# Performance work log

Measured on AMD Instinct MI355X. Metric: run time of the kernel, lower is better.

The kernel has to match this reference:

```python
import jax, jax.numpy as jnp
import numpy as np

B, S, D, H, E, K = 4, 1024, 1024, 4096, 8, 2

def setup_inputs() -> dict:
    key = jax.random.key(0)
    ks = jax.random.split(key, 6)
    sd = 1.0 / np.sqrt(D)
    sh = 1.0 / np.sqrt(H)
    return {
        "x": jax.random.normal(ks[0], (B, S, D), jnp.float32),
        "Wg": jax.random.normal(ks[1], (D, E), jnp.float32) * sd,
        "bg": jnp.zeros((E,), jnp.float32),
        "W1": jax.random.normal(ks[2], (E, D, H), jnp.float32) * sd,
        "b1": jnp.zeros((E, H), jnp.float32),
        "Wa": jax.random.normal(ks[3], (E, D, H), jnp.float32) * sd,
        "ba": jnp.zeros((E, H), jnp.float32),
        "W2": jax.random.normal(ks[4], (E, H, D), jnp.float32) * sh,
        "b2": jnp.zeros((E, D), jnp.float32),
        "kv_cache": 0,
    }

def reference(x, Wg, bg, W1, b1, Wa, ba, W2, b2, kv_cache):
    # gate: softmax over experts, top-k, renormalize
    gate = jax.nn.softmax(x @ Wg + bg, axis=-1)            # [B,S,E]
    w, idx = jax.lax.top_k(gate, K)                        # [B,S,K]
    w = w / jnp.sum(w, axis=-1, keepdims=True)
    # dense all-expert FF with SwiGLU: fc2( silu(fc_a(x)) * fc1(x) )
    a = jnp.einsum('bsd,edh->bseh', x, Wa) + ba            # [B,S,E,H]
    g = a * jax.nn.sigmoid(a)
    u = jnp.einsum('bsd,edh->bseh', x, W1) + b1
    y = jnp.einsum('bseh,ehd->bsed', g * u, W2) + b2       # [B,S,E,D]
    # gather top-k experts per token and combine
    sel = jnp.take_along_axis(y, idx[..., None], axis=2)   # [B,S,K,D]
    out = jnp.sum(sel * w[..., None], axis=-2)             # [B,S,D]
    return out
```

## Files before the change

kernel.cpp:

```cpp
#include <hip/hip_runtime.h>
#include <hip/hip_bf16.h>
#include <math.h>

#define TOKENS 4096
#define DD 1024
#define HH 4096
#define NE 8
#define PAIRS 8192
#define ROWCAP 8448
#define TILE_CAP 40

typedef __bf16 bf16x8 __attribute__((ext_vector_type(8)));
typedef float f32x4 __attribute__((ext_vector_type(4)));

__device__ __forceinline__ unsigned short f2bf(float f) {
  union { float f; unsigned int u; } c; c.f = f;
  unsigned int x = c.u;
  return (unsigned short)((x + 0x7fffu + ((x >> 16) & 1u)) >> 16);
}

__device__ __forceinline__ void lds16(void* l, const void* g) {
  __builtin_amdgcn_global_load_lds((const __attribute__((address_space(1))) void*)g,
                                   (__attribute__((address_space(3))) void*)l, 16, 0, 0);
}

__global__ void init_kernel(int* counts) {
  if (threadIdx.x < NE) counts[threadIdx.x] = 0;
}

__global__ __launch_bounds__(256) void transpose_kernel(const float* __restrict__ in,
                                                        unsigned short* __restrict__ out,
                                                        int R, int C) {
  int ntr = R >> 6, ntc = C >> 6;
  int per_e = ntr * ntc;
  int b = blockIdx.x;
  int e = b / per_e;
  int rem = b - e * per_e;
  int tr = rem / ntc, tc = rem - (rem / ntc) * ntc;
  const float* ie = in + (size_t)e * R * C;
  unsigned short* oe = out + (size_t)e * R * C;

  __shared__ float t[64][68];
  int tid = threadIdx.x;
  int lr = tid >> 2;
  int c4 = (tid & 3) << 4;
  const float* src = ie + (size_t)(tr * 64 + lr) * C + tc * 64 + c4;
  float4 v0 = *(const float4*)(src);
  float4 v1 = *(const float4*)(src + 4);
  float4 v2 = *(const float4*)(src + 8);
  float4 v3 = *(const float4*)(src + 12);
  *(float4*)&t[lr][c4] = v0;
  *(float4*)&t[lr][c4 + 4] = v1;
  *(float4*)&t[lr][c4 + 8] = v2;
  *(float4*)&t[lr][c4 + 12] = v3;
  __syncthreads();

  int oc = tid >> 2;
  int r0 = (tid & 3) << 4;
  unsigned int pk[8];
#pragma unroll
  for (int i = 0; i < 8; i++) {
    unsigned int lo = f2bf(t[r0 + 2 * i][oc]);
    unsigned int hi = f2bf(t[r0 + 2 * i + 1][oc]);
    pk[i] = lo | (hi << 16);
  }
  unsigned short* dst = oe + (size_t)(tc * 64 + oc) * R + tr * 64 + r0;
  *(uint4*)(dst) = make_uint4(pk[0], pk[1], pk[2], pk[3]);
  *(uint4*)(dst + 8) = make_uint4(pk[4], pk[5], pk[6], pk[7]);
}

__global__ __launch_bounds__(256) void gate_kernel(const float* __restrict__ x,
    const float* __restrict__ Wg, const float* __restrict__ bg,
    int* __restrict__ counts, int* __restrict__ tok_e, int* __restrict__ tok_slot,
    float* __restrict__ tok_w) {
  int t = blockIdx.x, tid = threadIdx.x;
  const float* xr = x + (size_t)t * DD;
  float p[8] = {0, 0, 0, 0, 0, 0, 0, 0};
  for (int d = tid; d < DD; d += 256) {
    float xv = xr[d];
    const float4* wrow = (const float4*)(Wg + (size_t)d * NE);
    float4 w0 = wrow[0], w1 = wrow[1];
    p[0] += xv * w0.x; p[1] += xv * w0.y; p[2] += xv * w0.z; p[3] += xv * w0.w;
    p[4] += xv * w1.x; p[5] += xv * w1.y; p[6] += xv * w1.z; p[7] += xv * w1.w;
  }
#pragma unroll
  for (int e = 0; e < 8; e++) {
    p[e] += __shfl_down(p[e], 32);
    p[e] += __shfl_down(p[e], 16);
    p[e] += __shfl_down(p[e], 8);
    p[e] += __shfl_down(p[e], 4);
    p[e] += __shfl_down(p[e], 2);
    p[e] += __shfl_down(p[e], 1);
  }
  __shared__ float red[4][8];
  if ((tid & 63) == 0) {
#pragma unroll
    for (int e = 0; e < 8; e++) red[tid >> 6][e] = p[e];
  }
  __syncthreads();
  if (tid == 0) {
    float l[8];
#pragma unroll
    for (int e = 0; e < 8; e++) l[e] = red[0][e] + red[1][e] + red[2][e] + red[3][e] + bg[e];
    int e0 = 0; float l0 = l[0];
    for (int e = 1; e < 8; e++) if (l[e] > l0) { e0 = e; l0 = l[e]; }
    int e1 = -1; float l1 = -3.4e38f;
    for (int e = 0; e < 8; e++) if (e != e0 && l[e] > l1) { e1 = e; l1 = l[e]; }
    float w0 = 1.f / (1.f + __expf(l1 - l0));
    float w1 = 1.f - w0;
    int s0 = atomicAdd(&counts[e0], 1);
    int s1 = atomicAdd(&counts[e1], 1);
    tok_e[2 * t] = e0;     tok_slot[2 * t] = s0;     tok_w[2 * t] = w0;
    tok_e[2 * t + 1] = e1; tok_slot[2 * t + 1] = s1; tok_w[2 * t + 1] = w1;
  }
}

__global__ void scan_kernel(const int* __restrict__ counts, int* __restrict__ offsets,
                            int* __restrict__ tm_e, int* __restrict__ tm_row0,
                            int* __restrict__ tm_nrow, int* __restrict__ ntp) {
  if (threadIdx.x != 0 || blockIdx.x != 0) return;
  int c[NE];
#pragma unroll
  for (int e = 0; e < NE; e++) c[e] = counts[e];
  int off = 0, nt = 0;
  for (int e = 0; e < NE; e++) {
    offsets[e] = off;
    for (int r = 0; r < c[e]; r += 256) {
      tm_e[nt] = e;
      tm_row0[nt] = off + r;
      tm_nrow[nt] = (c[e] - r < 256) ? (c[e] - r) : 256;
      nt++;
    }
    off += c[e];
  }
  *ntp = nt;
}

__global__ __launch_bounds__(64) void gather_kernel(const float* __restrict__ x,
    const int* __restrict__ tok_e, const int* __restrict__ tok_slot,
    const float* __restrict__ tok_w, const int* __restrict__ offsets,
    unsigned short* __restrict__ Xe, int* __restrict__ pair_row, float* __restrict__ rw) {
  int pp = blockIdx.x, tid = threadIdx.x;
  int e = tok_e[pp];
  int row = offsets[e] + tok_slot[pp];
  int t = pp >> 1;
  const float* src = x + (size_t)t * DD + tid * 16;
  float4 v0 = *(const float4*)(src);
  float4 v1 = *(const float4*)(src + 4);
  float4 v2 = *(const float4*)(src + 8);
  float4 v3 = *(const float4*)(src + 12);
  unsigned int pk[8];
  pk[0] = f2bf(v0.x) | ((unsigned int)f2bf(v0.y) << 16);
  pk[1] = f2bf(v0.z) | ((unsigned int)f2bf(v0.w) << 16);
  pk[2] = f2bf(v1.x) | ((unsigned int)f2bf(v1.y) << 16);
  pk[3] = f2bf(v1.z) | ((unsigned int)f2bf(v1.w) << 16);
  pk[4] = f2bf(v2.x) | ((unsigned int)f2bf(v2.y) << 16);
  pk[5] = f2bf(v2.z) | ((unsigned int)f2bf(v2.w) << 16);
  pk[6] = f2bf(v3.x) | ((unsigned int)f2bf(v3.y) << 16);
  pk[7] = f2bf(v3.z) | ((unsigned int)f2bf(v3.w) << 16);
  unsigned short* dst = Xe + (size_t)row * DD + tid * 16;
  *(uint4*)(dst) = make_uint4(pk[0], pk[1], pk[2], pk[3]);
  *(uint4*)(dst + 8) = make_uint4(pk[4], pk[5], pk[6], pk[7]);
  if (tid == 0) { pair_row[pp] = row; rw[row] = tok_w[pp]; }
}

__global__ __launch_bounds__(512, 2) void gemm1_kernel(
    const unsigned short* __restrict__ Xe,
    const unsigned short* __restrict__ WaT,
    const unsigned short* __restrict__ W1T,
    const float* __restrict__ ba, const float* __restrict__ b1,
    unsigned short* __restrict__ h,
    const int* __restrict__ tm_e, const int* __restrict__ tm_row0,
    const int* __restrict__ tm_nrow, const int* __restrict__ ntp) {
  extern __shared__ unsigned short sm[];
  int chunk = gridDim.x >> 3;
  int work = (blockIdx.x & 7) * chunk + (blockIdx.x >> 3);
  int tile = work >> 5;
  if (tile >= *ntp) return;
  int n0 = (work & 31) << 7;
  int e = tm_e[tile], row0 = tm_row0[tile], nrow = tm_nrow[tile];

  int tid = threadIdx.x;
  int lane = tid & 63, wid = tid >> 6;
  int wm = wid >> 2, wn = wid & 3;
  int fr = lane & 15, kc = lane >> 4;

  const unsigned short* gA = Xe + (size_t)row0 * DD;
  const unsigned short* gBa = WaT + ((size_t)e << 22) + (size_t)n0 * DD;
  const unsigned short* gBu = W1T + ((size_t)e << 22) + (size_t)n0 * DD;

  int sr = tid >> 2;
  int sk = (tid & 3) << 3;

  f32x4 accA[8][2], accU[8][2];
  f32x4 z = {0.f, 0.f, 0.f, 0.f};
#pragma unroll
  for (int m = 0; m < 8; m++)
#pragma unroll
    for (int n = 0; n < 2; n++) { accA[m][n] = z; accU[m][n] = z; }

  auto stage = [&](int kt, int buf) {
    int k0 = kt << 5;
    unsigned short* L = sm + buf * 16384;
    lds16(L + (size_t)tid * 8,         gA + (size_t)sr * DD + k0 + sk);
    lds16(L + (size_t)(tid + 512) * 8, gA + (size_t)(sr + 128) * DD + k0 + sk);
    lds16(L + 8192 + (size_t)tid * 8,  gBa + (size_t)sr * DD + k0 + sk);
    lds16(L + 12288 + (size_t)tid * 8, gBu + (size_t)sr * DD + k0 + sk);
  };

  stage(0, 0);
  for (int t = 0; t < 32; ++t) {
    int nxt = (t + 1 < 32) ? t + 1 : 31;
    stage(nxt, (t + 1) & 1);
    asm volatile("s_waitcnt vmcnt(4)\ns_barrier" ::: "memory");
    const unsigned short* L = sm + (t & 1) * 16384;
    bf16x8 a[8], bA[2], bU[2];
#pragma unroll
    for (int m = 0; m < 8; m++)
      a[m] = *(const bf16x8*)(L + (wm * 128 + m * 16 + fr) * 32 + kc * 8);
#pragma unroll
    for (int n = 0; n < 2; n++) {
      bA[n] = *(const bf16x8*)(L + 8192 + (wn * 32 + n * 16 + fr) * 32 + kc * 8);
      bU[n] = *(const bf16x8*)(L + 12288 + (wn * 32 + n * 16 + fr) * 32 + kc * 8);
    }
#pragma unroll
    for (int m = 0; m < 8; m++)
#pragma unroll
      for (int n = 0; n < 2; n++) {
        accA[m][n] = __builtin_amdgcn_mfma_f32_16x16x32_bf16(a[m], bA[n], accA[m][n], 0, 0, 0);
        accU[m][n] = __builtin_amdgcn_mfma_f32_16x16x32_bf16(a[m], bU[n], accU[m][n], 0, 0, 0);
      }
    asm volatile("s_waitcnt lgkmcnt(0)\ns_barrier" ::: "memory");
  }

  int lr4 = kc * 4;
#pragma unroll
  for (int n = 0; n < 2; n++) {
    int col = n0 + wn * 32 + n * 16 + fr;
    float bav = ba[e * HH + col];
    float buv = b1[e * HH + col];
#pragma unroll
    for (int m = 0; m < 8; m++) {
#pragma unroll
      for (int j = 0; j < 4; j++) {
        int r = wm * 128 + m * 16 + lr4 + j;
        if (r < nrow) {
          float av = accA[m][n][j] + bav;
          float uv = accU[m][n][j] + buv;
          float s = __builtin_amdgcn_rcpf(1.f + __expf(-av));
          float hv = av * s * uv;
          h[(size_t)(row0 + r) * HH + col] = f2bf(hv);
        }
      }
    }
  }
}

__global__ __launch_bounds__(512, 2) void gemm2_kernel(
    const unsigned short* __restrict__ h,
    const unsigned short* __restrict__ W2T,
    const float* __restrict__ b2, const float* __restrict__ rw,
    float* __restrict__ contrib,
    const int* __restrict__ tm_e, const int* __restrict__ tm_row0,
    const int* __restrict__ tm_nrow, const int* __restrict__ ntp) {
  extern __shared__ unsigned short sm[];
  int chunk = gridDim.x >> 3;
  int work = (blockIdx.x & 7) * chunk + (blockIdx.x >> 3);
  int tile = work >> 3;
  if (tile >= *ntp) return;
  int n0 = (work & 7) << 7;
  int e = tm_e[tile], row0 = tm_row0[tile], nrow = tm_nrow[tile];

  int tid = threadIdx.x;
  int lane = tid & 63, wid = tid >> 6;
  int wm = wid >> 1, wn = wid & 1;
  int fr = lane & 15, kc = lane >> 4;

  const unsigned short* gA = h + (size_t)row0 * HH;
  const unsigned short* gB = W2T + ((size_t)e << 22) + (size_t)n0 * HH;

  int sr = tid >> 2;
  int sk = (tid & 3) << 3;

  f32x4 acc[4][4];
  f32x4 z = {0.f, 0.f, 0.f, 0.f};
#pragma unroll
  for (int m = 0; m < 4; m++)
#pragma unroll
    for (int n = 0; n < 4; n++) acc[m][n] = z;

  auto stage = [&](int kt, int buf) {
    int k0 = kt << 5;
    unsigned short* L = sm + buf * 12288;
    lds16(L + (size_t)tid * 8,         gA + (size_t)sr * HH + k0 + sk);
    lds16(L + (size_t)(tid + 512) * 8, gA + (size_t)(sr + 128) * HH + k0 + sk);
    lds16(L + 8192 + (size_t)tid * 8,  gB + (size_t)sr * HH + k0 + sk);
  };

  stage(0, 0);
  for (int t = 0; t < 128; ++t) {
    int nxt = (t + 1 < 128) ? t + 1 : 127;
    stage(nxt, (t + 1) & 1);
    asm volatile("s_waitcnt vmcnt(3)\ns_barrier" ::: "memory");
    const unsigned short* L = sm + (t & 1) * 12288;
    bf16x8 a[4], b[4];
#pragma unroll
    for (int m = 0; m < 4; m++)
      a[m] = *(const bf16x8*)(L + (wm * 64 + m * 16 + fr) * 32 + kc * 8);
#pragma unroll
    for (int n = 0; n < 4; n++)
      b[n] = *(const bf16x8*)(L + 8192 + (wn * 64 + n * 16 + fr) * 32 + kc * 8);
#pragma unroll
    for (int m = 0; m < 4; m++)
#pragma unroll
      for (int n = 0; n < 4; n++)
        acc[m][n] = __builtin_amdgcn_mfma_f32_16x16x32_bf16(a[m], b[n], acc[m][n], 0, 0, 0);
    asm volatile("s_waitcnt lgkmcnt(0)\ns_barrier" ::: "memory");
  }

  float b2v[4];
#pragma unroll
  for (int n = 0; n < 4; n++) b2v[n] = b2[e * DD + n0 + wn * 64 + n * 16 + fr];
  int lr4 = kc * 4;
#pragma unroll
  for (int m = 0; m < 4; m++) {
#pragma unroll
    for (int j = 0; j < 4; j++) {
      int r = wm * 64 + m * 16 + lr4 + j;
      if (r < nrow) {
        float wv = rw[row0 + r];
        float* dst = contrib + (size_t)(row0 + r) * DD + n0 + wn * 64 + fr;
#pragma unroll
        for (int n = 0; n < 4; n++)
          dst[n * 16] = wv * (acc[m][n][j] + b2v[n]);
      }
    }
  }
}

__global__ __launch_bounds__(256) void combine_kernel(const float* __restrict__ contrib,
    const int* __restrict__ pair_row, float* __restrict__ out) {
  int t = blockIdx.x, tid = threadIdx.x;
  int r0 = pair_row[2 * t], r1 = pair_row[2 * t + 1];
  const float4* c0 = (const float4*)(contrib + (size_t)r0 * DD);
  const float4* c1 = (const float4*)(contrib + (size_t)r1 * DD);
  float4* o = (float4*)(out + (size_t)t * DD);
  float4 a = c0[tid], b = c1[tid];
  o[tid] = make_float4(a.x + b.x, a.y + b.y, a.z + b.z, a.w + b.w);
}

extern "C" void kernel_launch(void* const* d_in, const int* in_sizes, int n_in,
                              void* d_out, int out_size, void* d_ws, size_t ws_size,
                              hipStream_t stream) {
  const float* x  = (const float*)d_in[0];
  const float* Wg = (const float*)d_in[1];
  const float* bg = (const float*)d_in[2];
  const float* W1 = (const float*)d_in[3];
  const float* b1 = (const float*)d_in[4];
  const float* Wa = (const float*)d_in[5];
  const float* ba = (const float*)d_in[6];
  const float* W2 = (const float*)d_in[7];
  const float* b2 = (const float*)d_in[8];
  float* out = (float*)d_out;
  (void)in_sizes; (void)n_in; (void)out_size; (void)ws_size;

  char* p = (char*)d_ws;
  auto take = [&](size_t bytes) { char* r = p; p += (bytes + 255) & ~(size_t)255; return r; };
  unsigned short* WaT = (unsigned short*)take((size_t)NE * HH * DD * 2);
  unsigned short* W1T = (unsigned short*)take((size_t)NE * HH * DD * 2);
  unsigned short* W2T = (unsigned short*)take((size_t)NE * DD * HH * 2);
  unsigned short* Xe  = (unsigned short*)take((size_t)ROWCAP * DD * 2);
  unsigned short* hb  = (unsigned short*)take((size_t)ROWCAP * HH * 2);
  float* contrib      = (float*)take((size_t)ROWCAP * DD * 4);
  int* counts   = (int*)take(64);
  int* offsets  = (int*)take(64);
  int* tok_e    = (int*)take(PAIRS * 4);
  int* tok_slot = (int*)take(PAIRS * 4);
  float* tok_w  = (float*)take(PAIRS * 4);
  int* pair_row = (int*)take(PAIRS * 4);
  float* rw     = (float*)take(ROWCAP * 4);
  int* tm_e     = (int*)take(TILE_CAP * 4);
  int* tm_row0  = (int*)take(TILE_CAP * 4);
  int* tm_nrow  = (int*)take(TILE_CAP * 4);
  int* ntp      = (int*)take(64);

  init_kernel<<<1, 64, 0, stream>>>(counts);
  transpose_kernel<<<NE * 16 * 64, 256, 0, stream>>>(Wa, WaT, DD, HH);
  transpose_kernel<<<NE * 16 * 64, 256, 0, stream>>>(W1, W1T, DD, HH);
  transpose_kernel<<<NE * 64 * 16, 256, 0, stream>>>(W2, W2T, HH, DD);
  gate_kernel<<<TOKENS, 256, 0, stream>>>(x, Wg, bg, counts, tok_e, tok_slot, tok_w);
  scan_kernel<<<1, 64, 0, stream>>>(counts, offsets, tm_e, tm_row0, tm_nrow, ntp);
  gather_kernel<<<PAIRS, 64, 0, stream>>>(x, tok_e, tok_slot, tok_w, offsets, Xe, pair_row, rw);
  gemm1_kernel<<<TILE_CAP * 32, 512, 64 * 1024, stream>>>(Xe, WaT, W1T, ba, b1, hb, tm_e, tm_row0, tm_nrow, ntp);
  gemm2_kernel<<<TILE_CAP * 8, 512, 48 * 1024, stream>>>(hb, W2T, b2, rw, contrib, tm_e, tm_row0, tm_nrow, ntp);
  combine_kernel<<<TOKENS, 256, 0, stream>>>(contrib, pair_row, out);
}
```

Before: 586.3 us.

## Restructure expert GEMMs with K=64 swizzled LDS tiles, interleaved prefetch and split-K

Both expert GEMMs now stage 64-wide K chunks into XOR-swizzled LDS slots and interleave partial MFMA groups with staggered global-to-LDS prefetches under s_setprio. The aim is to cut LDS bank conflicts and hide load latency better. gemm2 gains a 2-way split-K, with the second half written to a buffer that reuses the WaT workspace and summed in the combine kernel. The block-index swizzle is dropped, and the reuse of WaT is only safe because gemm1 finishes before gemm2 on the stream.

```diff
diff --git a/kernel.cpp b/kernel.cpp
--- a/kernel.cpp
+++ b/kernel.cpp
@@ -9,6 +9,8 @@
 #define PAIRS 8192
 #define ROWCAP 8448
 #define TILE_CAP 40
+#define G1_NT 16
+#define G2_NT 32
 
 typedef __bf16 bf16x8 __attribute__((ext_vector_type(8)));
 typedef float f32x4 __attribute__((ext_vector_type(4)));
@@ -172,9 +174,9 @@
     unsigned short* __restrict__ h,
     const int* __restrict__ tm_e, const int* __restrict__ tm_row0,
     const int* __restrict__ tm_nrow, const int* __restrict__ ntp) {
-  extern __shared__ unsigned short sm[];
-  int chunk = gridDim.x >> 3;
-  int work = (blockIdx.x & 7) * chunk + (blockIdx.x >> 3);
+  __shared__ unsigned short sm[8][8192];
+
+  int work = blockIdx.x;
   int tile = work >> 5;
   if (tile >= *ntp) return;
   int n0 = (work & 31) << 7;
@@ -185,12 +187,25 @@
   int wm = wid >> 2, wn = wid & 3;
   int fr = lane & 15, kc = lane >> 4;
 
-  const unsigned short* gA = Xe + (size_t)row0 * DD;
+  const unsigned short* gA  = Xe + (size_t)row0 * DD;
+  const unsigned short* gA1 = gA + (size_t)128 * DD;
   const unsigned short* gBa = WaT + ((size_t)e << 22) + (size_t)n0 * DD;
   const unsigned short* gBu = W1T + ((size_t)e << 22) + (size_t)n0 * DD;
 
-  int sr = tid >> 2;
-  int sk = (tid & 3) << 3;
+  int srow = tid >> 3;
+  int sx0 = (((tid & 7) ^ (srow & 7)) << 3);
+
+  auto stg = [&](int tt, int slot, const unsigned short* gsrc) {
+    int c = tt < G1_NT ? tt : G1_NT - 1;
+    unsigned short* L = &sm[((tt & 1) << 2) | slot][0];
+    const unsigned short* s = gsrc + (size_t)srow * DD + (c << 6) + sx0;
+    lds16(L + (size_t)tid * 8, s);
+    lds16(L + (size_t)(tid + 512) * 8, s + (size_t)64 * DD);
+  };
+  auto fragp = [&](int buf, int slot, int r, int ks) {
+    return (const bf16x8*)(&sm[(buf << 2) | slot][0] + r * 64 +
+                           ((((ks << 2) | kc) ^ (r & 7)) << 3));
+  };
 
   f32x4 accA[8][2], accU[8][2];
   f32x4 z = {0.f, 0.f, 0.f, 0.f};
@@ -199,38 +214,81 @@
 #pragma unroll
     for (int n = 0; n < 2; n++) { accA[m][n] = z; accU[m][n] = z; }
 
-  auto stage = [&](int kt, int buf) {
-    int k0 = kt << 5;
-    unsigned short* L = sm + buf * 16384;
-    lds16(L + (size_t)tid * 8,         gA + (size_t)sr * DD + k0 + sk);
-    lds16(L + (size_t)(tid + 512) * 8, gA + (size_t)(sr + 128) * DD + k0 + sk);
-    lds16(L + 8192 + (size_t)tid * 8,  gBa + (size_t)sr * DD + k0 + sk);
-    lds16(L + 12288 + (size_t)tid * 8, gBu + (size_t)sr * DD + k0 + sk);
-  };
-
-  stage(0, 0);
-  for (int t = 0; t < 32; ++t) {
-    int nxt = (t + 1 < 32) ? t + 1 : 31;
-    stage(nxt, (t + 1) & 1);
-    asm volatile("s_waitcnt vmcnt(4)\ns_barrier" ::: "memory");
-    const unsigned short* L = sm + (t & 1) * 16384;
-    bf16x8 a[8], bA[2], bU[2];
-#pragma unroll
-    for (int m = 0; m < 8; m++)
-      a[m] = *(const bf16x8*)(L + (wm * 128 + m * 16 + fr) * 32 + kc * 8);
-#pragma unroll
-    for (int n = 0; n < 2; n++) {
-      bA[n] = *(const bf16x8*)(L + 8192 + (wn * 32 + n * 16 + fr) * 32 + kc * 8);
-      bU[n] = *(const bf16x8*)(L + 12288 + (wn * 32 + n * 16 + fr) * 32 + kc * 8);
-    }
-#pragma unroll
-    for (int m = 0; m < 8; m++)
-#pragma unroll
-      for (int n = 0; n < 2; n++) {
-        accA[m][n] = __builtin_amdgcn_mfma_f32_16x16x32_bf16(a[m], bA[n], accA[m][n], 0, 0, 0);
-        accU[m][n] = __builtin_amdgcn_mfma_f32_16x16x32_bf16(a[m], bU[n], accU[m][n], 0, 0, 0);
+  stg(0, 2, gBa); stg(0, 3, gBu); stg(0, 0, gA); stg(0, 1, gA1);
+  stg(1, 2, gBa); stg(1, 3, gBu); stg(1, 0, gA);
+  asm volatile("s_waitcnt vmcnt(6)\ns_barrier" ::: "memory");
+
+  for (int T = 0; T < G1_NT; ++T) {
+    int buf = T & 1;
+    bf16x8 a[4][2], bA[2][2], bU[2][2];
+#pragma unroll
+    for (int m = 0; m < 4; m++)
+#pragma unroll
+      for (int ks = 0; ks < 2; ks++) {
+        int R = wm * 128 + m * 16 + fr;
+        a[m][ks] = *fragp(buf, R >> 7, R & 127, ks);
       }
+#pragma unroll
+    for (int n = 0; n < 2; n++)
+#pragma unroll
+      for (int ks = 0; ks < 2; ks++)
+        bA[n][ks] = *fragp(buf, 2, wn * 32 + n * 16 + fr, ks);
+    stg(T + 1, 1, gA1);
+    __builtin_amdgcn_s_setprio(1);
+#pragma unroll
+    for (int m = 0; m < 4; m++)
+#pragma unroll
+      for (int n = 0; n < 2; n++)
+#pragma unroll
+        for (int ks = 0; ks < 2; ks++)
+          accA[m][n] = __builtin_amdgcn_mfma_f32_16x16x32_bf16(a[m][ks], bA[n][ks], accA[m][n], 0, 0, 0);
+    __builtin_amdgcn_s_setprio(0);
     asm volatile("s_waitcnt lgkmcnt(0)\ns_barrier" ::: "memory");
+#pragma unroll
+    for (int n = 0; n < 2; n++)
+#pragma unroll
+      for (int ks = 0; ks < 2; ks++)
+        bU[n][ks] = *fragp(buf, 3, wn * 32 + n * 16 + fr, ks);
+    stg(T + 2, 2, gBa);
+    __builtin_amdgcn_s_setprio(1);
+#pragma unroll
+    for (int m = 0; m < 4; m++)
+#pragma unroll
+      for (int n = 0; n < 2; n++)
+#pragma unroll
+        for (int ks = 0; ks < 2; ks++)
+          accU[m][n] = __builtin_amdgcn_mfma_f32_16x16x32_bf16(a[m][ks], bU[n][ks], accU[m][n], 0, 0, 0);
+    __builtin_amdgcn_s_setprio(0);
+    asm volatile("s_waitcnt lgkmcnt(0)\ns_barrier" ::: "memory");
+#pragma unroll
+    for (int m = 0; m < 4; m++)
+#pragma unroll
+      for (int ks = 0; ks < 2; ks++) {
+        int R = wm * 128 + 64 + m * 16 + fr;
+        a[m][ks] = *fragp(buf, R >> 7, R & 127, ks);
+      }
+    stg(T + 2, 3, gBu);
+    __builtin_amdgcn_s_setprio(1);
+#pragma unroll
+    for (int m = 0; m < 4; m++)
+#pragma unroll
+      for (int n = 0; n < 2; n++)
+#pragma unroll
+        for (int ks = 0; ks < 2; ks++)
+          accA[4 + m][n] = __builtin_amdgcn_mfma_f32_16x16x32_bf16(a[m][ks], bA[n][ks], accA[4 + m][n], 0, 0, 0);
+    __builtin_amdgcn_s_setprio(0);
+    asm volatile("s_waitcnt lgkmcnt(0)\ns_barrier" ::: "memory");
+    stg(T + 2, 0, gA);
+    __builtin_amdgcn_s_setprio(1);
+#pragma unroll
+    for (int m = 0; m < 4; m++)
+#pragma unroll
+      for (int n = 0; n < 2; n++)
+#pragma unroll
+        for (int ks = 0; ks < 2; ks++)
+          accU[4 + m][n] = __builtin_amdgcn_mfma_f32_16x16x32_bf16(a[m][ks], bU[n][ks], accU[4 + m][n], 0, 0, 0);
+    __builtin_amdgcn_s_setprio(0);
+    asm volatile("s_waitcnt vmcnt(6)\ns_barrier" ::: "memory");
   }
 
   int lr4 = kc * 4;
@@ -248,8 +306,7 @@
           float av = accA[m][n][j] + bav;
           float uv = accU[m][n][j] + buv;
           float s = __builtin_amdgcn_rcpf(1.f + __expf(-av));
-          float hv = av * s * uv;
-          h[(size_t)(row0 + r) * HH + col] = f2bf(hv);
+          h[(size_t)(row0 + r) * HH + col] = f2bf(av * s * uv);
         }
       }
     }
@@ -257,96 +314,146 @@
 }
 
 __global__ __launch_bounds__(512, 2) void gemm2_kernel(
-    const unsigned short* __restrict__ h,
+    const unsigned short* __restrict__ hb,
     const unsigned short* __restrict__ W2T,
     const float* __restrict__ b2, const float* __restrict__ rw,
-    float* __restrict__ contrib,
+    float* __restrict__ contribA, float* __restrict__ contribB,
     const int* __restrict__ tm_e, const int* __restrict__ tm_row0,
     const int* __restrict__ tm_nrow, const int* __restrict__ ntp) {
-  extern __shared__ unsigned short sm[];
-  int chunk = gridDim.x >> 3;
-  int work = (blockIdx.x & 7) * chunk + (blockIdx.x >> 3);
-  int tile = work >> 3;
+  __shared__ unsigned short sm[9][8192];
+
+  int work = blockIdx.x;
+  int tile = work >> 4;
   if (tile >= *ntp) return;
-  int n0 = (work & 7) << 7;
+  int rem = work & 15;
+  int n0 = (rem >> 1) << 7;
+  int kh = rem & 1;
   int e = tm_e[tile], row0 = tm_row0[tile], nrow = tm_nrow[tile];
 
   int tid = threadIdx.x;
   int lane = tid & 63, wid = tid >> 6;
-  int wm = wid >> 1, wn = wid & 1;
+  int wm = wid >> 2, wn = wid & 3;
   int fr = lane & 15, kc = lane >> 4;
 
-  const unsigned short* gA = h + (size_t)row0 * HH;
-  const unsigned short* gB = W2T + ((size_t)e << 22) + (size_t)n0 * HH;
-
-  int sr = tid >> 2;
-  int sk = (tid & 3) << 3;
-
-  f32x4 acc[4][4];
+  const unsigned short* gA = hb + (size_t)row0 * HH + kh * 2048;
+  const unsigned short* gB = W2T + ((size_t)e << 22) + (size_t)n0 * HH + kh * 2048;
+
+  int srow = tid >> 3;
+  int sx0 = (((tid & 7) ^ (srow & 7)) << 3);
+
+  auto stgA = [&](int tt) {
+    int c = tt < G2_NT ? tt : G2_NT - 1;
+    int sl = (tt % 3) << 1;
+    const unsigned short* s = gA + (size_t)srow * HH + (c << 6) + sx0;
+    lds16(&sm[sl][0] + (size_t)tid * 8, s);
+    lds16(&sm[sl][0] + (size_t)(tid + 512) * 8, s + (size_t)64 * HH);
+    lds16(&sm[sl + 1][0] + (size_t)tid * 8, s + (size_t)128 * HH);
+    lds16(&sm[sl + 1][0] + (size_t)(tid + 512) * 8, s + (size_t)192 * HH);
+  };
+  auto stgB = [&](int tt) {
+    int c = tt < G2_NT ? tt : G2_NT - 1;
+    unsigned short* L = &sm[6 + tt % 3][0];
+    const unsigned short* s = gB + (size_t)srow * HH + (c << 6) + sx0;
+    lds16(L + (size_t)tid * 8, s);
+    lds16(L + (size_t)(tid + 512) * 8, s + (size_t)64 * HH);
+  };
+  auto fragp = [&](int slot, int r, int ks) {
+    return (const bf16x8*)(&sm[slot][0] + r * 64 + ((((ks << 2) | kc) ^ (r & 7)) << 3));
+  };
+
+  f32x4 acc[8][2];
   f32x4 z = {0.f, 0.f, 0.f, 0.f};
 #pragma unroll
-  for (int m = 0; m < 4; m++)
-#pragma unroll
-    for (int n = 0; n < 4; n++) acc[m][n] = z;
-
-  auto stage = [&](int kt, int buf) {
-    int k0 = kt << 5;
-    unsigned short* L = sm + buf * 12288;
-    lds16(L + (size_t)tid * 8,         gA + (size_t)sr * HH + k0 + sk);
-    lds16(L + (size_t)(tid + 512) * 8, gA + (size_t)(sr + 128) * HH + k0 + sk);
-    lds16(L + 8192 + (size_t)tid * 8,  gB + (size_t)sr * HH + k0 + sk);
-  };
-
-  stage(0, 0);
-  for (int t = 0; t < 128; ++t) {
-    int nxt = (t + 1 < 128) ? t + 1 : 127;
-    stage(nxt, (t + 1) & 1);
-    asm volatile("s_waitcnt vmcnt(3)\ns_barrier" ::: "memory");
-    const unsigned short* L = sm + (t & 1) * 12288;
-    bf16x8 a[4], b[4];
-#pragma unroll
-    for (int m = 0; m < 4; m++)
-      a[m] = *(const bf16x8*)(L + (wm * 64 + m * 16 + fr) * 32 + kc * 8);
-#pragma unroll
-    for (int n = 0; n < 4; n++)
-      b[n] = *(const bf16x8*)(L + 8192 + (wn * 64 + n * 16 + fr) * 32 + kc * 8);
-#pragma unroll
-    for (int m = 0; m < 4; m++)
-#pragma unroll
-      for (int n = 0; n < 4; n++)
-        acc[m][n] = __builtin_amdgcn_mfma_f32_16x16x32_bf16(a[m], b[n], acc[m][n], 0, 0, 0);
+  for (int m = 0; m < 8; m++)
+#pragma unroll
+    for (int n = 0; n < 2; n++) acc[m][n] = z;
+
+  stgB(0); stgA(0); stgB(1); stgA(1); stgB(2);
+  asm volatile("s_waitcnt vmcnt(6)\ns_barrier" ::: "memory");
+
+  for (int T = 0; T < G2_NT; ++T) {
+    int slA = (T % 3) << 1;
+    int slB = 6 + T % 3;
+    bf16x8 a[4][2], b[2][2];
+#pragma unroll
+    for (int m = 0; m < 4; m++)
+#pragma unroll
+      for (int ks = 0; ks < 2; ks++) {
+        int R = wm * 128 + m * 16 + fr;
+        a[m][ks] = *fragp(slA + (R >> 7), R & 127, ks);
+      }
+#pragma unroll
+    for (int n = 0; n < 2; n++)
+#pragma unroll
+      for (int ks = 0; ks < 2; ks++)
+        b[n][ks] = *fragp(slB, wn * 32 + n * 16 + fr, ks);
+    stgA(T + 2);
+    __builtin_amdgcn_s_setprio(1);
+#pragma unroll
+    for (int m = 0; m < 4; m++)
+#pragma unroll
+      for (int n = 0; n < 2; n++)
+#pragma unroll
+        for (int ks = 0; ks < 2; ks++)
+          acc[m][n] = __builtin_amdgcn_mfma_f32_16x16x32_bf16(a[m][ks], b[n][ks], acc[m][n], 0, 0, 0);
+    __builtin_amdgcn_s_setprio(0);
     asm volatile("s_waitcnt lgkmcnt(0)\ns_barrier" ::: "memory");
-  }
-
-  float b2v[4];
-#pragma unroll
-  for (int n = 0; n < 4; n++) b2v[n] = b2[e * DD + n0 + wn * 64 + n * 16 + fr];
+#pragma unroll
+    for (int m = 0; m < 4; m++)
+#pragma unroll
+      for (int ks = 0; ks < 2; ks++) {
+        int R = wm * 128 + 64 + m * 16 + fr;
+        a[m][ks] = *fragp(slA + (R >> 7), R & 127, ks);
+      }
+    stgB(T + 3);
+    __builtin_amdgcn_s_setprio(1);
+#pragma unroll
+    for (int m = 0; m < 4; m++)
+#pragma unroll
+      for (int n = 0; n < 2; n++)
+#pragma unroll
+        for (int ks = 0; ks < 2; ks++)
+          acc[4 + m][n] = __builtin_amdgcn_mfma_f32_16x16x32_bf16(a[m][ks], b[n][ks], acc[4 + m][n], 0, 0, 0);
+    __builtin_amdgcn_s_setprio(0);
+    asm volatile("s_waitcnt vmcnt(6) lgkmcnt(0)\ns_barrier" ::: "memory");
+  }
+
+  float b2v[2];
+#pragma unroll
+  for (int n = 0; n < 2; n++)
+    b2v[n] = (kh == 0) ? b2[e * DD + n0 + wn * 32 + n * 16 + fr] : 0.f;
+  float* cbuf = kh ? contribB : contribA;
   int lr4 = kc * 4;
 #pragma unroll
-  for (int m = 0; m < 4; m++) {
+  for (int m = 0; m < 8; m++) {
 #pragma unroll
     for (int j = 0; j < 4; j++) {
-      int r = wm * 64 + m * 16 + lr4 + j;
+      int r = wm * 128 + m * 16 + lr4 + j;
       if (r < nrow) {
         float wv = rw[row0 + r];
-        float* dst = contrib + (size_t)(row0 + r) * DD + n0 + wn * 64 + fr;
-#pragma unroll
-        for (int n = 0; n < 4; n++)
-          dst[n * 16] = wv * (acc[m][n][j] + b2v[n]);
+        float* dst = cbuf + (size_t)(row0 + r) * DD + n0 + wn * 32 + fr;
+        dst[0]  = wv * (acc[m][0][j] + b2v[0]);
+        dst[16] = wv * (acc[m][1][j] + b2v[1]);
       }
     }
   }
 }
 
-__global__ __launch_bounds__(256) void combine_kernel(const float* __restrict__ contrib,
-    const int* __restrict__ pair_row, float* __restrict__ out) {
+__global__ __launch_bounds__(256) void combine_kernel(const float* __restrict__ cA,
+    const float* __restrict__ cB, const int* __restrict__ pair_row,
+    float* __restrict__ out) {
   int t = blockIdx.x, tid = threadIdx.x;
   int r0 = pair_row[2 * t], r1 = pair_row[2 * t + 1];
-  const float4* c0 = (const float4*)(contrib + (size_t)r0 * DD);
-  const float4* c1 = (const float4*)(contrib + (size_t)r1 * DD);
+  const float4* a0 = (const float4*)(cA + (size_t)r0 * DD);
+  const float4* b0 = (const float4*)(cB + (size_t)r0 * DD);
+  const float4* a1 = (const float4*)(cA + (size_t)r1 * DD);
+  const float4* b1 = (const float4*)(cB + (size_t)r1 * DD);
   float4* o = (float4*)(out + (size_t)t * DD);
-  float4 a = c0[tid], b = c1[tid];
-  o[tid] = make_float4(a.x + b.x, a.y + b.y, a.z + b.z, a.w + b.w);
+  float4 x0 = a0[tid], y0 = b0[tid], x1 = a1[tid], y1 = b1[tid];
+  o[tid] = make_float4((x0.x + y0.x) + (x1.x + y1.x),
+                       (x0.y + y0.y) + (x1.y + y1.y),
+                       (x0.z + y0.z) + (x1.z + y1.z),
+                       (x0.w + y0.w) + (x1.w + y1.w));
 }
 
 extern "C" void kernel_launch(void* const* d_in, const int* in_sizes, int n_in,
@@ -371,7 +478,7 @@
   unsigned short* W2T = (unsigned short*)take((size_t)NE * DD * HH * 2);
   unsigned short* Xe  = (unsigned short*)take((size_t)ROWCAP * DD * 2);
   unsigned short* hb  = (unsigned short*)take((size_t)ROWCAP * HH * 2);
-  float* contrib      = (float*)take((size_t)ROWCAP * DD * 4);
+  float* contribA     = (float*)take((size_t)ROWCAP * DD * 4);
   int* counts   = (int*)take(64);
   int* offsets  = (int*)take(64);
   int* tok_e    = (int*)take(PAIRS * 4);
@@ -383,6 +490,7 @@
   int* tm_row0  = (int*)take(TILE_CAP * 4);
   int* tm_nrow  = (int*)take(TILE_CAP * 4);
   int* ntp      = (int*)take(64);
+  float* contribB = (float*)WaT;
 
   init_kernel<<<1, 64, 0, stream>>>(counts);
   transpose_kernel<<<NE * 16 * 64, 256, 0, stream>>>(Wa, WaT, DD, HH);
@@ -391,7 +499,7 @@
   gate_kernel<<<TOKENS, 256, 0, stream>>>(x, Wg, bg, counts, tok_e, tok_slot, tok_w);
   scan_kernel<<<1, 64, 0, stream>>>(counts, offsets, tm_e, tm_row0, tm_nrow, ntp);
   gather_kernel<<<PAIRS, 64, 0, stream>>>(x, tok_e, tok_slot, tok_w, offsets, Xe, pair_row, rw);
-  gemm1_kernel<<<TILE_CAP * 32, 512, 64 * 1024, stream>>>(Xe, WaT, W1T, ba, b1, hb, tm_e, tm_row0, tm_nrow, ntp);
-  gemm2_kernel<<<TILE_CAP * 8, 512, 48 * 1024, stream>>>(hb, W2T, b2, rw, contrib, tm_e, tm_row0, tm_nrow, ntp);
-  combine_kernel<<<TOKENS, 256, 0, stream>>>(contrib, pair_row, out);
-}
+  gemm1_kernel<<<TILE_CAP * 32, 512, 0, stream>>>(Xe, WaT, W1T, ba, b1, hb, tm_e, tm_row0, tm_nrow, ntp);
+  gemm2_kernel<<<TILE_CAP * 16, 512, 0, stream>>>(hb, W2T, b2, rw, contribA, contribB, tm_e, tm_row0, tm_nrow, ntp);
+  combine_kernel<<<TOKENS, 256, 0, stream>>>(contribA, contribB, pair_row, out);
+}
```

Result: faster. 533.4 us (-9.0%).
